# Optimization experiments

Hardware: AMD Instinct MI355X
Metric: run time of the kernel (lower is better)

## Reference

```python
import jax, jax.numpy as jnp
import numpy as np

B, S, D = 4, 2048, 1024
H, HD = 16, 64
F = 4096
EPS = 1e-5


def layer_norm(x, gamma, beta):
    mu = jnp.mean(x, axis=-1, keepdims=True)
    var = jnp.var(x, axis=-1, keepdims=True)
    return (x - mu) * jax.lax.rsqrt(var + EPS) * gamma + beta


def setup_inputs() -> dict:
    key = jax.random.key(0)
    ks = jax.random.split(key, 16)
    s_d = 1.0 / np.sqrt(D)
    s_hd = 1.0 / np.sqrt(H * HD)
    s_f = 1.0 / np.sqrt(F)
    return {
        "x": jax.random.normal(ks[0], (B, S, D), jnp.float32),
        # per-head Q/K/V linears stacked over heads: [H, D, HD]
        "Wq": jax.random.uniform(ks[1], (H, D, HD), jnp.float32, -s_d, s_d),
        "bq": jax.random.uniform(ks[2], (H, HD), jnp.float32, -s_d, s_d),
        "Wk": jax.random.uniform(ks[3], (H, D, HD), jnp.float32, -s_d, s_d),
        "bk": jax.random.uniform(ks[4], (H, HD), jnp.float32, -s_d, s_d),
        "Wv": jax.random.uniform(ks[5], (H, D, HD), jnp.float32, -s_d, s_d),
        "bv": jax.random.uniform(ks[6], (H, HD), jnp.float32, -s_d, s_d),
        "Wo": jax.random.uniform(ks[7], (H * HD, D), jnp.float32, -s_hd, s_hd),
        "bo": jax.random.uniform(ks[8], (D,), jnp.float32, -s_hd, s_hd),
        "W1": jax.random.uniform(ks[9], (D, F), jnp.float32, -s_d, s_d),
        "b1": jax.random.uniform(ks[10], (F,), jnp.float32, -s_d, s_d),
        "W2": jax.random.uniform(ks[11], (F, D), jnp.float32, -s_f, s_f),
        "b2": jax.random.uniform(ks[12], (D,), jnp.float32, -s_f, s_f),
        "g1": jnp.ones((D,), jnp.float32),
        "be1": jnp.zeros((D,), jnp.float32),
        "g2": jnp.ones((D,), jnp.float32),
        "be2": jnp.zeros((D,), jnp.float32),
    }


def reference(x, Wq, bq, Wk, bk, Wv, bv, Wo, bo, W1, b1, W2, b2, g1, be1, g2, be2):
    scale = HD ** (-0.5)
    # per-head projections: [B,S,H,HD]
    Q = jnp.einsum("bsd,hde->bshe", x, Wq) + bq
    K = jnp.einsum("bsd,hde->bshe", x, Wk) + bk
    V = jnp.einsum("bsd,hde->bshe", x, Wv) + bv
    scores = jnp.einsum("bqhe,bkhe->bhqk", Q, K) * scale
    attn = jax.nn.softmax(scores, axis=-1)
    ctx = jnp.einsum("bhqk,bkhe->bqhe", attn, V)  # [B,S,H,HD]
    concat = ctx.reshape(B, S, H * HD)  # head-order concat
    attn_out = concat @ Wo + bo
    x1 = layer_norm(x + attn_out, g1, be1)
    ffn = jax.nn.relu(x1 @ W1 + b1) @ W2 + b2
    return layer_norm(x1 + ffn, g2, be2)
```

## Files before the change

kernel.cpp:

```cpp
#include <hip/hip_runtime.h>

#define B_ 4
#define S_ 2048
#define D_ 1024
#define H_ 16
#define HD_ 64
#define F_ 4096
#define M_ (B_*S_)
#define QS_ 3072


typedef __attribute__((ext_vector_type(8))) short bf16x8;
typedef __attribute__((ext_vector_type(4))) short short4_t;
typedef __attribute__((ext_vector_type(4))) float f32x4;
typedef __attribute__((ext_vector_type(16))) float f32x16;

#define AS1q __attribute__((address_space(1)))
#define AS3q __attribute__((address_space(3)))

__device__ __forceinline__ float bf2f(short u) {
    union { unsigned int i; float f; } v;
    v.i = ((unsigned int)(unsigned short)u) << 16;
    return v.f;
}
__device__ __forceinline__ short f2bf(float f) {
    union { float f; unsigned int i; } v; v.f = f;
    unsigned int r = v.i + 0x7fffu + ((v.i >> 16) & 1u);
    return (short)(r >> 16);
}
__device__ __forceinline__ void gld_lds16(const short* g, short* l) {
    __builtin_amdgcn_global_load_lds((const AS1q void*)g, (AS3q void*)l, 16, 0, 0);
}
__device__ __forceinline__ unsigned int cvtpk_bf16(float a, float b) {
    unsigned int r;
    asm("v_cvt_pk_bf16_f32 %0, %1, %2" : "=v"(r) : "v"(a), "v"(b));
    return r;
}
__device__ __forceinline__ float max3f(float a, float b, float c) {
    float r;
    asm("v_max3_f32 %0, %1, %2, %3" : "=v"(r) : "v"(a), "v"(b), "v"(c));
    return r;
}

__global__ __launch_bounds__(256) void cvt_f2b_k(
    const float* __restrict__ in, short* __restrict__ out, long n)
{
    long i = ((long)blockIdx.x * 256 + threadIdx.x) * 4;
    long stride = (long)gridDim.x * 256 * 4;
    for (; i < n; i += stride) {
        float4 v = *(const float4*)(in + i);
        short4_t o;
        o[0] = f2bf(v.x); o[1] = f2bf(v.y); o[2] = f2bf(v.z); o[3] = f2bf(v.w);
        *(short4_t*)(out + i) = o;
    }
}

template<typename TI>
__global__ __launch_bounds__(256) void transpose_k(
    const TI* __restrict__ in, short* __restrict__ out,
    int rows, long in_rstride,
    long in_bstrideB, long in_bstrideH, long out_bstride)
{
    __shared__ short tile[32][33];
    int z = blockIdx.z;
    const TI* ip = in + (long)(z >> 4) * in_bstrideB + (long)(z & 15) * in_bstrideH;
    short* op = out + (long)z * out_bstride;
    int r0 = blockIdx.y * 32, c0 = blockIdx.x * 32;
    int tx = threadIdx.x & 31, ty = threadIdx.x >> 5;
#pragma unroll
    for (int i = 0; i < 32; i += 8) {
        TI v = ip[(long)(r0 + ty + i) * in_rstride + (c0 + tx)];
        if constexpr (sizeof(TI) == 4) tile[ty + i][tx] = f2bf((float)v);
        else                           tile[ty + i][tx] = (short)v;
    }
    __syncthreads();
#pragma unroll
    for (int i = 0; i < 32; i += 8)
        op[(long)(c0 + ty + i) * rows + (r0 + tx)] = tile[tx][ty + i];
}

__global__ __launch_bounds__(256) void gemm_k(
    const short* __restrict__ A,
    const short* __restrict__ BT,
    const float* __restrict__ bias,
    short* __restrict__ C,
    int M, int N, int K, float scale, int relu)
{
    __shared__ short Alds[128*32];
    __shared__ short Blds[128*32];
    int tid = threadIdx.x;
    int wave = tid >> 6, lane = tid & 63;
    int lgrp = lane >> 4, lrow = lane & 15;
    int wr = wave >> 1, wc = wave & 1;
    int gx = gridDim.x;
    int nwg = gx * gridDim.y;
    int lin = blockIdx.y * gx + blockIdx.x;
    int nid = (lin & 7) * (nwg >> 3) + (lin >> 3);
    int bm = (nid / gx) * 128, bn = (nid % gx) * 128;

    int srow = wave * 32 + (lane >> 2);
    int scol = (lane & 3) * 8;
    const short* gA = A  + (long)(bm + srow) * K + scol;
    const short* gB = BT + (long)(bn + srow) * K + scol;
    short* lA0 = &Alds[(wave * 32) * 32];
    short* lA1 = &Alds[(wave * 32 + 16) * 32];
    short* lB0 = &Blds[(wave * 32) * 32];
    short* lB1 = &Blds[(wave * 32 + 16) * 32];
    long k16 = 16L * K;

    f32x4 acc[4][4] = {};
    for (int k0 = 0; k0 < K; k0 += 32) {
        gld_lds16(gA + k0,       lA0);
        gld_lds16(gA + k0 + k16, lA1);
        gld_lds16(gB + k0,       lB0);
        gld_lds16(gB + k0 + k16, lB1);
        __syncthreads();
        bf16x8 af[4], bv[4];
#pragma unroll
        for (int i = 0; i < 4; i++) {
            af[i] = *(const bf16x8*)&Alds[(wr*64 + i*16 + lrow) * 32 + 8*lgrp];
            bv[i] = *(const bf16x8*)&Blds[(wc*64 + i*16 + lrow) * 32 + 8*lgrp];
        }
#pragma unroll
        for (int mi = 0; mi < 4; mi++)
#pragma unroll
            for (int ni = 0; ni < 4; ni++)
                acc[mi][ni] = __builtin_amdgcn_mfma_f32_16x16x32_bf16(
                    af[mi], bv[ni], acc[mi][ni], 0, 0, 0);
        __syncthreads();
    }
#pragma unroll
    for (int ni = 0; ni < 4; ni++) {
        int col = bn + wc*64 + ni*16 + lrow;
        float bb = bias[col];
#pragma unroll
        for (int mi = 0; mi < 4; mi++) {
#pragma unroll
            for (int j = 0; j < 4; j++) {
                int row = bm + wr*64 + mi*16 + lgrp*4 + j;
                float v = (acc[mi][ni][j] + bb) * scale;
                if (relu) v = fmaxf(v, 0.0f);
                C[(long)row * N + col] = f2bf(v);
            }
        }
    }
}

__global__ __launch_bounds__(256) void gemm_qkv_k(
    const short* __restrict__ A,
    const short* __restrict__ BT,
    const float* __restrict__ bq,
    const float* __restrict__ bk,
    const float* __restrict__ bv,
    short* __restrict__ C,
    float qscale)
{
    __shared__ short Alds[128*32];
    __shared__ short Blds[128*32];
    const int K = 1024;
    int tid = threadIdx.x;
    int wave = tid >> 6, lane = tid & 63;
    int lgrp = lane >> 4, lrow = lane & 15;
    int wr = wave >> 1, wc = wave & 1;
    int gx = gridDim.x;
    int nwg = gx * gridDim.y;
    int lin = blockIdx.y * gx + blockIdx.x;
    int nid = (lin & 7) * (nwg >> 3) + (lin >> 3);
    int bm = (nid / gx) * 128, bn = (nid % gx) * 128;
    int seg = bn >> 10;
    const float* bp = (seg == 0) ? bq : (seg == 1) ? bk : bv;
    float scale = (seg == 0) ? qscale : 1.0f;

    int srow = wave * 32 + (lane >> 2);
    int scol = (lane & 3) * 8;
    const short* gA = A  + (long)(bm + srow) * K + scol;
    const short* gB = BT + (long)(bn + srow) * K + scol;
    short* lA0 = &Alds[(wave * 32) * 32];
    short* lA1 = &Alds[(wave * 32 + 16) * 32];
    short* lB0 = &Blds[(wave * 32) * 32];
    short* lB1 = &Blds[(wave * 32 + 16) * 32];
    long k16 = 16L * K;

    f32x4 acc[4][4] = {};
    for (int k0 = 0; k0 < K; k0 += 32) {
        gld_lds16(gA + k0,       lA0);
        gld_lds16(gA + k0 + k16, lA1);
        gld_lds16(gB + k0,       lB0);
        gld_lds16(gB + k0 + k16, lB1);
        __syncthreads();
        bf16x8 af[4], bvv[4];
#pragma unroll
        for (int i = 0; i < 4; i++) {
            af[i]  = *(const bf16x8*)&Alds[(wr*64 + i*16 + lrow) * 32 + 8*lgrp];
            bvv[i] = *(const bf16x8*)&Blds[(wc*64 + i*16 + lrow) * 32 + 8*lgrp];
        }
#pragma unroll
        for (int mi = 0; mi < 4; mi++)
#pragma unroll
            for (int ni = 0; ni < 4; ni++)
                acc[mi][ni] = __builtin_amdgcn_mfma_f32_16x16x32_bf16(
                    af[mi], bvv[ni], acc[mi][ni], 0, 0, 0);
        __syncthreads();
    }
#pragma unroll
    for (int ni = 0; ni < 4; ni++) {
        int col = bn + wc*64 + ni*16 + lrow;
        float bb = bp[col & 1023];
#pragma unroll
        for (int mi = 0; mi < 4; mi++) {
#pragma unroll
            for (int j = 0; j < 4; j++) {
                int row = bm + wr*64 + mi*16 + lgrp*4 + j;
                C[(long)row * QS_ + col] = f2bf((acc[mi][ni][j] + bb) * scale);
            }
        }
    }
}

__global__ __launch_bounds__(256) void attn_k(
    const short* __restrict__ QKV,
    const short* __restrict__ VT,
    short* __restrict__ O)
{
    __shared__ short KV[2][2][4096];
    int lin = blockIdx.y * 16 + blockIdx.x;
    int nid = (lin & 7) * 128 + (lin >> 3);
    int bh = nid >> 4, qt = nid & 15;
    int b = bh >> 4, h = bh & 15;
    int q0 = qt * 128;
    int tid = threadIdx.x, wave = tid >> 6, lane = tid & 63;
    int l31 = lane & 31, hi = lane >> 5;
    int sw = l31 & 7;

    bf16x8 aq[4];
    {
        const short* qp = QKV + (long)(b*S_ + q0 + wave*32 + l31) * QS_ + h*64 + 8*hi;
#pragma unroll
        for (int t = 0; t < 4; t++)
            aq[t] = *(const bf16x8*)(qp + 16*t);
    }
    bf16x8 ones;
#pragma unroll
    for (int i = 0; i < 8; i++) ones[i] = (short)0x3F80;

    f32x16 accO[2] = {};
    f32x16 accsum = {};
    float mj = -1e30f;

    int srow = lane >> 3;
    int schunk = (lane & 7) ^ srow;
    const short* ksrc = QKV + (long)(b*S_ + wave*16 + srow) * QS_ + 1024 + h*64 + schunk*8;
    const short* vsrc = VT + (long)bh * (64L*S_) + (long)(wave*16 + srow) * S_ + schunk*8;
    short* kd = &KV[0][0][wave*1024];
    short* vd = &KV[0][1][wave*1024];

    #define STAGE(buf, kb_) do {                                        \
        gld_lds16(ksrc + (long)(kb_)     * QS_, kd + (buf)*8192);        \
        gld_lds16(ksrc + (long)((kb_)+8) * QS_, kd + (buf)*8192 + 512);  \
        gld_lds16(vsrc + (kb_),                 vd + (buf)*8192);        \
        gld_lds16(vsrc + 8*S_ + (kb_),          vd + (buf)*8192 + 512);  \
    } while (0)

    STAGE(0, 0);
    __syncthreads();

    for (int t = 0; t < 32; ++t) {
        int cur = t & 1;
        if (t < 31) STAGE(cur ^ 1, (t + 1) * 64);
        const char* KB = (const char*)&KV[cur][0][0];
        const char* VB = (const char*)&KV[cur][1][0];

        f32x16 accs[2] = {};
#pragma unroll
        for (int c = 0; c < 2; c++) {
            bf16x8 ak[4];
#pragma unroll
            for (int tt = 0; tt < 4; tt++)
                ak[tt] = *(const bf16x8*)(KB + (32*c + l31)*128 + (((2*tt + hi) ^ sw) << 4));
            __builtin_amdgcn_s_setprio(1);
#pragma unroll
            for (int tt = 0; tt < 4; tt++)
                accs[c] = __builtin_amdgcn_mfma_f32_32x32x16_bf16(
                    ak[tt], aq[tt], accs[c], 0, 0, 0);
            __builtin_amdgcn_s_setprio(0);
        }

        float mA = fmaxf(accs[0][0], accs[0][1]);
        float mB = fmaxf(accs[1][0], accs[1][1]);
#pragma unroll
        for (int r = 2; r < 16; r += 2) {
            mA = max3f(mA, accs[0][r], accs[0][r+1]);
            mB = max3f(mB, accs[1][r], accs[1][r+1]);
        }
        float m4 = fmaxf(mA, mB);
        if (!__all(m4 <= mj + 8.0f)) {
            float m2 = fmaxf(m4, __shfl_xor(m4, 32));
            float mnew = fmaxf(mj, m2);
            float al = exp2f(mj - mnew);
            mj = mnew;
#pragma unroll
            for (int r = 0; r < 16; r++) {
                float alr = __shfl(al, (r & 3) + 8 * (r >> 2) + 4 * hi);
                accO[0][r] *= alr; accO[1][r] *= alr; accsum[r] *= alr;
            }
        }
#pragma unroll
        for (int c = 0; c < 2; c++)
#pragma unroll
            for (int r = 0; r < 16; r++)
                accs[c][r] = exp2f(accs[c][r] - mj);

        bf16x8 pa[4];
#pragma unroll
        for (int ks = 0; ks < 4; ks++) {
            int c = ks >> 1, o = (ks & 1) * 8;
            unsigned int c0 = cvtpk_bf16(accs[c][o+0], accs[c][o+1]);
            unsigned int c1 = cvtpk_bf16(accs[c][o+2], accs[c][o+3]);
            unsigned int c2 = cvtpk_bf16(accs[c][o+4], accs[c][o+5]);
            unsigned int c3 = cvtpk_bf16(accs[c][o+6], accs[c][o+7]);
            asm("v_permlane32_swap_b32 %0, %1" : "+v"(c0), "+v"(c2));
            asm("v_permlane32_swap_b32 %0, %1" : "+v"(c1), "+v"(c3));
            union { unsigned int u[4]; bf16x8 v; } pk;
            pk.u[0] = c0; pk.u[1] = c1; pk.u[2] = c2; pk.u[3] = c3;
            pa[ks] = pk.v;
        }

        __builtin_amdgcn_s_setprio(1);
#pragma unroll
        for (int eb = 0; eb < 2; eb++)
#pragma unroll
            for (int ks = 0; ks < 4; ks++) {
                bf16x8 bvf = *(const bf16x8*)(VB + (32*eb + l31)*128 + (((2*ks + hi) ^ sw) << 4));
                accO[eb] = __builtin_amdgcn_mfma_f32_32x32x16_bf16(
                    pa[ks], bvf, accO[eb], 0, 0, 0);
            }
#pragma unroll
        for (int ks = 0; ks < 4; ks++)
            accsum = __builtin_amdgcn_mfma_f32_32x32x16_bf16(
                pa[ks], ones, accsum, 0, 0, 0);
        __builtin_amdgcn_s_setprio(0);

        __syncthreads();
    }
    #undef STAGE

    const short* ob = O + (long)(b*S_) * 1024 + h*64;
#pragma unroll
    for (int r = 0; r < 16; r++) {
        int crow = (r & 3) + 8 * (r >> 2) + 4 * hi;
        float invr = 1.0f / accsum[r];
        int qr = q0 + wave*32 + crow;
#pragma unroll
        for (int eb = 0; eb < 2; eb++)
            ((short*)ob)[(long)qr * 1024 + 32*eb + l31] = f2bf(accO[eb][r] * invr);
    }
}

template<int XF32, int OUTF32>
__global__ __launch_bounds__(256) void ln_k(
    const void* __restrict__ Xv, const short* __restrict__ Y,
    const float* __restrict__ g, const float* __restrict__ be,
    void* __restrict__ Ov)
{
    int row = blockIdx.x, tid = threadIdx.x;
    long base = (long)row * 1024 + tid * 4;
    float a[4];
    if constexpr (XF32) {
        float4 xv = *(const float4*)((const float*)Xv + base);
        a[0] = xv.x; a[1] = xv.y; a[2] = xv.z; a[3] = xv.w;
    } else {
        short4_t xv = *(const short4_t*)((const short*)Xv + base);
#pragma unroll
        for (int j = 0; j < 4; j++) a[j] = bf2f(xv[j]);
    }
    short4_t yv = *(const short4_t*)(Y + base);
    float s = 0.f, s2 = 0.f;
#pragma unroll
    for (int j = 0; j < 4; j++) {
        a[j] += bf2f(yv[j]);
        s += a[j]; s2 += a[j] * a[j];
    }
#pragma unroll
    for (int off = 32; off >= 1; off >>= 1) {
        s  += __shfl_xor(s, off);
        s2 += __shfl_xor(s2, off);
    }
    __shared__ float red[8];
    if ((tid & 63) == 0) { red[(tid >> 6)*2] = s; red[(tid >> 6)*2 + 1] = s2; }
    __syncthreads();
    s  = red[0] + red[2] + red[4] + red[6];
    s2 = red[1] + red[3] + red[5] + red[7];
    float mean = s * (1.0f/1024.0f);
    float var  = s2 * (1.0f/1024.0f) - mean*mean;
    float rstd = rsqrtf(var + 1e-5f);
    float4 gv = *(const float4*)(g  + tid*4);
    float4 bv = *(const float4*)(be + tid*4);
    float r0 = (a[0] - mean) * rstd * gv.x + bv.x;
    float r1 = (a[1] - mean) * rstd * gv.y + bv.y;
    float r2 = (a[2] - mean) * rstd * gv.z + bv.z;
    float r3 = (a[3] - mean) * rstd * gv.w + bv.w;
    if constexpr (OUTF32) {
        *(float4*)((float*)Ov + base) = make_float4(r0, r1, r2, r3);
    } else {
        short4_t ov;
        ov[0] = f2bf(r0); ov[1] = f2bf(r1); ov[2] = f2bf(r2); ov[3] = f2bf(r3);
        *(short4_t*)((short*)Ov + base) = ov;
    }
}

extern "C" void kernel_launch(void* const* d_in, const int* in_sizes, int n_in,
                              void* d_out, int out_size, void* d_ws, size_t ws_size,
                              hipStream_t stream)
{
    static const int ins[17] = {0,1,2,3,4,5,6,7,8,9,10,11,12,13,14,15,16};
    static const int srt[17] = {16,4,12,2,10,5,13,3,11,0,6,1,7,14,8,15,9};
    const int* IX = (in_sizes[0] == 8388608) ? ins : srt;

    const float* x   = (const float*)d_in[IX[0]];
    const float* Wq  = (const float*)d_in[IX[1]];
    const float* bq  = (const float*)d_in[IX[2]];
    const float* Wk  = (const float*)d_in[IX[3]];
    const float* bk  = (const float*)d_in[IX[4]];
    const float* Wv  = (const float*)d_in[IX[5]];
    const float* bv  = (const float*)d_in[IX[6]];
    const float* Wo  = (const float*)d_in[IX[7]];
    const float* bo  = (const float*)d_in[IX[8]];
    const float* W1  = (const float*)d_in[IX[9]];
    const float* b1  = (const float*)d_in[IX[10]];
    const float* W2  = (const float*)d_in[IX[11]];
    const float* b2  = (const float*)d_in[IX[12]];
    const float* g1  = (const float*)d_in[IX[13]];
    const float* be1 = (const float*)d_in[IX[14]];
    const float* g2  = (const float*)d_in[IX[15]];
    const float* be2 = (const float*)d_in[IX[16]];
    short* ws  = (short*)d_ws;

    short* QKVb = ws + 0L;
    short* VTb  = ws + 25165824L;
    short* ctx  = ws + 33554432L;
    short* QKVT = ws + 41943040L;
    short* WoT  = ws + 45088768L;
    short* xb   = ws + 46137344L;
    short* W1T  = ws + 54525952L;
    short* W2T  = ws + 58720256L;
    short* x1   = ws + 0L;
    short* hb   = ws + 8388608L;
    short* ao   = ws + 46137344L;
    short* ffn  = ws + 41943040L;

    dim3 blk(256);

    cvt_f2b_k<<<2048, blk, 0, stream>>>(x, xb, (long)M_ * D_);

    transpose_k<float><<<dim3(2, 32, 16),  blk, 0, stream>>>(Wq, QKVT,            1024, 64,   0, 65536, 65536);
    transpose_k<float><<<dim3(2, 32, 16),  blk, 0, stream>>>(Wk, QKVT + 1048576L, 1024, 64,   0, 65536, 65536);
    transpose_k<float><<<dim3(2, 32, 16),  blk, 0, stream>>>(Wv, QKVT + 2097152L, 1024, 64,   0, 65536, 65536);
    transpose_k<float><<<dim3(32, 32, 1),  blk, 0, stream>>>(Wo, WoT, 1024, 1024, 0, 0, 0);
    transpose_k<float><<<dim3(128, 32, 1), blk, 0, stream>>>(W1, W1T, 1024, 4096, 0, 0, 0);
    transpose_k<float><<<dim3(32, 128, 1), blk, 0, stream>>>(W2, W2T, 4096, 1024, 0, 0, 0);

    gemm_qkv_k<<<dim3(24, 64), blk, 0, stream>>>(
        xb, QKVT, bq, bk, bv, QKVb, 0.18033688011112042f);

    transpose_k<short><<<dim3(2, 64, 64), blk, 0, stream>>>(
        QKVb + 2048, VTb, 2048, QS_, (long)S_*QS_, 64, 131072);

    attn_k<<<dim3(16, 64), blk, 0, stream>>>(QKVb, VTb, ctx);

    gemm_k<<<dim3(8, 64), blk, 0, stream>>>(ctx, WoT, bo, ao, M_, 1024, 1024, 1.0f, 0);
    ln_k<1,0><<<8192, blk, 0, stream>>>(x, ao, g1, be1, x1);

    gemm_k<<<dim3(32, 64), blk, 0, stream>>>(x1, W1T, b1, hb,  M_, 4096, 1024, 1.0f, 1);
    gemm_k<<<dim3(8, 64),  blk, 0, stream>>>(hb, W2T, b2, ffn, M_, 1024, 4096, 1.0f, 0);

    ln_k<0,1><<<8192, blk, 0, stream>>>(x1, ffn, g2, be2, d_out);
}
```

Baseline: 470.1 us.

## Double-buffer LDS tiles in GEMM kernels to overlap global loads with MFMA

Both the generic GEMM and the fused QKV GEMM now keep two LDS buffers for the A and B tiles. The loads for the next K-step are issued into the idle buffer before the MFMA work on the current buffer. This removes one of the two barriers per K-step and is meant to hide global-to-LDS latency behind compute. The cost is double the LDS per workgroup, which may lower occupancy.

```diff
diff --git a/kernel.cpp b/kernel.cpp
--- a/kernel.cpp
+++ b/kernel.cpp
@@ -86,8 +86,8 @@
     short* __restrict__ C,
     int M, int N, int K, float scale, int relu)
 {
-    __shared__ short Alds[128*32];
-    __shared__ short Blds[128*32];
+    __shared__ short Alds[2*128*32];
+    __shared__ short Blds[2*128*32];
     int tid = threadIdx.x;
     int wave = tid >> 6, lane = tid & 63;
     int lgrp = lane >> 4, lrow = lane & 15;
@@ -108,18 +108,25 @@
     short* lB1 = &Blds[(wave * 32 + 16) * 32];
     long k16 = 16L * K;
 
+    #define GSTAGE(buf, k0_) do {                              \
+        gld_lds16(gA + (k0_),       lA0 + (buf)*4096);         \
+        gld_lds16(gA + (k0_) + k16, lA1 + (buf)*4096);         \
+        gld_lds16(gB + (k0_),       lB0 + (buf)*4096);         \
+        gld_lds16(gB + (k0_) + k16, lB1 + (buf)*4096);         \
+    } while (0)
+
     f32x4 acc[4][4] = {};
-    for (int k0 = 0; k0 < K; k0 += 32) {
-        gld_lds16(gA + k0,       lA0);
-        gld_lds16(gA + k0 + k16, lA1);
-        gld_lds16(gB + k0,       lB0);
-        gld_lds16(gB + k0 + k16, lB1);
-        __syncthreads();
+    int nk = K >> 5;
+    GSTAGE(0, 0);
+    __syncthreads();
+    for (int t = 0; t < nk; ++t) {
+        int cur = t & 1;
+        if (t + 1 < nk) GSTAGE(cur ^ 1, (t + 1) * 32);
         bf16x8 af[4], bv[4];
 #pragma unroll
         for (int i = 0; i < 4; i++) {
-            af[i] = *(const bf16x8*)&Alds[(wr*64 + i*16 + lrow) * 32 + 8*lgrp];
-            bv[i] = *(const bf16x8*)&Blds[(wc*64 + i*16 + lrow) * 32 + 8*lgrp];
+            af[i] = *(const bf16x8*)&Alds[cur*4096 + (wr*64 + i*16 + lrow) * 32 + 8*lgrp];
+            bv[i] = *(const bf16x8*)&Blds[cur*4096 + (wc*64 + i*16 + lrow) * 32 + 8*lgrp];
         }
 #pragma unroll
         for (int mi = 0; mi < 4; mi++)
@@ -129,6 +136,7 @@
                     af[mi], bv[ni], acc[mi][ni], 0, 0, 0);
         __syncthreads();
     }
+    #undef GSTAGE
 #pragma unroll
     for (int ni = 0; ni < 4; ni++) {
         int col = bn + wc*64 + ni*16 + lrow;
@@ -155,8 +163,8 @@
     short* __restrict__ C,
     float qscale)
 {
-    __shared__ short Alds[128*32];
-    __shared__ short Blds[128*32];
+    __shared__ short Alds[2*128*32];
+    __shared__ short Blds[2*128*32];
     const int K = 1024;
     int tid = threadIdx.x;
     int wave = tid >> 6, lane = tid & 63;
@@ -181,18 +189,24 @@
     short* lB1 = &Blds[(wave * 32 + 16) * 32];
     long k16 = 16L * K;
 
+    #define GSTAGE(buf, k0_) do {                              \
+        gld_lds16(gA + (k0_),       lA0 + (buf)*4096);         \
+        gld_lds16(gA + (k0_) + k16, lA1 + (buf)*4096);         \
+        gld_lds16(gB + (k0_),       lB0 + (buf)*4096);         \
+        gld_lds16(gB + (k0_) + k16, lB1 + (buf)*4096);         \
+    } while (0)
+
     f32x4 acc[4][4] = {};
-    for (int k0 = 0; k0 < K; k0 += 32) {
-        gld_lds16(gA + k0,       lA0);
-        gld_lds16(gA + k0 + k16, lA1);
-        gld_lds16(gB + k0,       lB0);
-        gld_lds16(gB + k0 + k16, lB1);
-        __syncthreads();
+    GSTAGE(0, 0);
+    __syncthreads();
+    for (int t = 0; t < 32; ++t) {
+        int cur = t & 1;
+        if (t < 31) GSTAGE(cur ^ 1, (t + 1) * 32);
         bf16x8 af[4], bvv[4];
 #pragma unroll
         for (int i = 0; i < 4; i++) {
-            af[i]  = *(const bf16x8*)&Alds[(wr*64 + i*16 + lrow) * 32 + 8*lgrp];
-            bvv[i] = *(const bf16x8*)&Blds[(wc*64 + i*16 + lrow) * 32 + 8*lgrp];
+            af[i]  = *(const bf16x8*)&Alds[cur*4096 + (wr*64 + i*16 + lrow) * 32 + 8*lgrp];
+            bvv[i] = *(const bf16x8*)&Blds[cur*4096 + (wc*64 + i*16 + lrow) * 32 + 8*lgrp];
         }
 #pragma unroll
         for (int mi = 0; mi < 4; mi++)
@@ -202,6 +216,7 @@
                     af[mi], bvv[ni], acc[mi][ni], 0, 0, 0);
         __syncthreads();
     }
+    #undef GSTAGE
 #pragma unroll
     for (int ni = 0; ni < 4; ni++) {
         int col = bn + wc*64 + ni*16 + lrow;
```

New measurement: 445.9 us. -5.1%, faster.
